# Kernel optimization log

Hardware: AMD Instinct MI355X
Metric: run time of the kernel (lower is better)

## Reference

```python
import jax, jax.numpy as jnp
import numpy as np
from jax import lax

B, N, C_IN, C_OUT = 4, 8192, 64, 128
STRIDE, RADIUS, K, L = 4, 0.1, 32, 2
EPS = 1e-5
M = N // STRIDE


def _bn(x, g, b):
    # training-mode batch norm, channel-first layout (B, C, ...)
    axes = (0,) + tuple(range(2, x.ndim))
    mean = jnp.mean(x, axis=axes, keepdims=True)
    var = jnp.mean((x - mean) ** 2, axis=axes, keepdims=True)
    sh = (1, -1) + (1,) * (x.ndim - 2)
    return (x - mean) * lax.rsqrt(var + EPS) * g.reshape(sh) + b.reshape(sh)


def _fps(points, m):
    # farthest point sampling starting at index 0 (matches fps_cuda semantics)
    b, n, _ = points.shape
    bi = jnp.arange(b)

    def body(carry, _):
        dis, last = carry
        lp = points[bi, last]  # (b,3)
        d = jnp.sum((points - lp[:, None, :]) ** 2, -1)
        dis = jnp.minimum(dis, d)
        return (dis, jnp.argmax(dis, -1).astype(jnp.int32)), last

    init = (jnp.full((b, n), 1e10, points.dtype), jnp.zeros((b,), jnp.int32))
    _, idx = lax.scan(body, init, None, length=m)
    return idx.T  # (b, m)


def _ball_query(radius, k, centroids, points, features):
    # first k points within radius of each centroid; pad with first hit
    b, n, _ = points.shape
    d2 = jnp.sum((centroids[:, :, None, :] - points[:, None, :, :]) ** 2, -1)  # (b,m,n)
    key = jnp.where(d2 < radius * radius, jnp.arange(n, dtype=jnp.int32), n)
    neg, _ = lax.top_k(-key, k)  # k smallest keys = first k in-ball indices
    sel = -neg  # (b,m,k)
    sel = jnp.where(sel == n, sel[..., :1], sel)
    sel = jnp.clip(sel, 0, n - 1)
    bi = jnp.arange(b)[:, None, None]
    gp = jnp.transpose(points[bi, sel], (0, 3, 2, 1))  # (b,3,k,m)
    gf = None
    if features is not None:
        gf = jnp.transpose(features[bi, sel], (0, 3, 2, 1))  # (b,c,k,m)
    return gp, gf


def _forward(pos, x, p):
    b, n, _ = pos.shape
    m = n // STRIDE
    bi = jnp.arange(b)[:, None]
    fps_idx = _fps(pos, m)
    centroids = pos[bi, fps_idx]  # (b,m,3)
    # x_mlp: 1x1 conv + BN + ReLU
    f = jax.nn.relu(_bn(jnp.einsum('bnc,oc->bon', x, p['W_x']), p['g_x'], p['b_x']))
    feats = jnp.transpose(f, (0, 2, 1))  # (b,n,C_OUT)
    gp, gf = _ball_query(RADIUS, K, centroids, pos, feats)
    cT = jnp.transpose(centroids, (0, 2, 1))[:, :, None, :]  # (b,3,1,m)
    gp = (gp - cT) / RADIUS
    gp = jax.nn.relu(_bn(jnp.einsum('bckm,oc->bokm', gp, p['W_ps']), p['g_ps'], p['b_ps']))
    xf = jnp.transpose(jnp.max(gf + gp, axis=2), (0, 2, 1))  # (b,m,C_OUT)
    # gen_pe on downsampled points
    R2 = RADIUS * 2
    gpe, _ = _ball_query(R2, K, centroids, centroids, None)
    gpe = (gpe - cT) / R2
    pe = jax.nn.relu(_bn(jnp.einsum('bckm,oc->bokm', gpe, p['W_pe']), p['g_pe'], p['b_pe']))
    # InvResMLP blocks
    for i in range(L):
        xc = jnp.transpose(xf, (0, 2, 1))  # (b,C,m)
        xc = jax.nn.relu(_bn(jnp.einsum('bcm,oc->bom', xc, p['W1'][i]), p['g1'][i], p['b1'][i]))
        feats_i = jnp.transpose(xc, (0, 2, 1))  # (b,m,C)
        _, gfi = _ball_query(R2, K, centroids, centroids, feats_i)
        g = jnp.max(gfi + pe, axis=2)  # (b,C,m)
        g = jax.nn.relu(_bn(jnp.einsum('bcm,oc->bom', g, p['W2a'][i]), p['g2a'][i], p['b2a'][i]))
        g = _bn(jnp.einsum('bcm,oc->bom', g, p['W2b'][i]), p['g2b'][i], p['b2b'][i])
        xf = jax.nn.relu(feats_i + jnp.transpose(g, (0, 2, 1)))
    return centroids, xf


def setup_inputs() -> dict:
    key = jax.random.key(0)
    ks = jax.random.split(key, 12)
    d = {
        'pos': jax.random.uniform(ks[0], (B, N, 3), jnp.float32),
        'x': jax.random.normal(ks[1], (B, N, C_IN), jnp.float32),
        'W_x': jax.random.normal(ks[2], (C_OUT, C_IN), jnp.float32) * 0.05,
        'g_x': jnp.ones((C_OUT,), jnp.float32), 'b_x': jnp.zeros((C_OUT,), jnp.float32),
        'W_ps': jax.random.normal(ks[3], (C_OUT, 3), jnp.float32) * 0.1,
        'g_ps': jnp.ones((C_OUT,), jnp.float32), 'b_ps': jnp.zeros((C_OUT,), jnp.float32),
        'W_pe': jax.random.normal(ks[4], (C_OUT, 3), jnp.float32) * 0.1,
        'g_pe': jnp.ones((C_OUT,), jnp.float32), 'b_pe': jnp.zeros((C_OUT,), jnp.float32),
        'W1': jax.random.normal(ks[5], (L, C_OUT, C_OUT), jnp.float32) * 0.05,
        'g1': jnp.ones((L, C_OUT), jnp.float32), 'b1': jnp.zeros((L, C_OUT), jnp.float32),
        'W2a': jax.random.normal(ks[6], (L, C_OUT, C_OUT), jnp.float32) * 0.05,
        'g2a': jnp.ones((L, C_OUT), jnp.float32), 'b2a': jnp.zeros((L, C_OUT), jnp.float32),
        'W2b': jax.random.normal(ks[7], (L, C_OUT, C_OUT), jnp.float32) * 0.05,
        'g2b': jnp.ones((L, C_OUT), jnp.float32), 'b2b': jnp.zeros((L, C_OUT), jnp.float32),
    }
    return d


def reference(pos, x, W_x, g_x, b_x, W_ps, g_ps, b_ps, W_pe, g_pe, b_pe,
              W1, g1, b1, W2a, g2a, b2a, W2b, g2b, b2b):
    p = dict(W_x=W_x, g_x=g_x, b_x=b_x, W_ps=W_ps, g_ps=g_ps, b_ps=b_ps,
             W_pe=W_pe, g_pe=g_pe, b_pe=b_pe, W1=W1, g1=g1, b1=b1,
             W2a=W2a, g2a=g2a, b2a=b2a, W2b=W2b, g2b=g2b, b2b=b2b)
    return _forward(pos, x, p)
```

## Files before the change

kernel.cpp:

```cpp
#include <hip/hip_runtime.h>


#define BB 4
#define NN 8192
#define MM 2048
#define HM 1024
#define KK 32
#define CI 64
#define CO 128
#define SG 16
#define CAPH 192

typedef float vf2 __attribute__((ext_vector_type(2)));

#define ST_X 0
#define MO_PS 256
#define MO_PE 272
#define ST1 288
#define ST2A (288 + 2 * SG * 256)
#define ST2B (ST2A + 2 * SG * 256)
#define ST_TOTAL (ST2B + 512)

__device__ __forceinline__ float sq3(float dx, float dy, float dz) {
#pragma clang fp contract(off)
  return dx * dx + dy * dy + dz * dz;
}

__device__ __forceinline__ void fin_stats_d(const double* st, float gam,
                                            float bet, double cnt, int ch,
                                            float* sc, float* sh) {
  double mean = st[ch] / cnt;
  double var = st[128 + ch] / cnt - mean * mean;
  if (var < 0) var = 0;
  double s = (double)gam / sqrt(var + 1e-5);
  *sc = (float)s;
  *sh = (float)((double)bet - mean * s);
}

__device__ __forceinline__ void fin_grp_d(const double* st, float gam,
                                          float bet, double cnt, int ch,
                                          float* sc, float* sh) {
  double sum = 0, ssq = 0;
#pragma unroll
  for (int g = 0; g < SG; g++) {
    sum += st[g * 256 + ch];
    ssq += st[g * 256 + 128 + ch];
  }
  double mean = sum / cnt;
  double var = ssq / cnt - mean * mean;
  if (var < 0) var = 0;
  double s = (double)gam / sqrt(var + 1e-5);
  *sc = (float)s;
  *sh = (float)((double)bet - mean * s);
}

__device__ __forceinline__ void fin_mom_d(const double* mo, const float* Wrow,
                                          float gam, float bet, double cnt,
                                          float* sc, float* sh) {
  double w0 = Wrow[0], w1 = Wrow[1], w2 = Wrow[2];
  double mx = mo[0] / cnt, my = mo[1] / cnt, mz = mo[2] / cnt;
  double sxx = mo[3] / cnt, sxy = mo[4] / cnt, sxz = mo[5] / cnt;
  double syy = mo[6] / cnt, syz = mo[7] / cnt, szz = mo[8] / cnt;
  double mean = w0 * mx + w1 * my + w2 * mz;
  double ey2 = w0 * w0 * sxx + w1 * w1 * syy + w2 * w2 * szz +
               2.0 * (w0 * w1 * sxy + w0 * w2 * sxz + w1 * w2 * syz);
  double var = ey2 - mean * mean;
  if (var < 0) var = 0;
  double s = (double)gam / sqrt(var + 1e-5);
  *sc = (float)s;
  *sh = (float)((double)bet - mean * s);
}

template <int CTRL>
__device__ __forceinline__ int dpp_i(int v) {
  return __builtin_amdgcn_update_dpp(v, v, CTRL, 0xF, 0xF, false);
}
template <int CTRL>
__device__ __forceinline__ float dpp_f(float v) {
  return __int_as_float(dpp_i<CTRL>(__float_as_int(v)));
}

#define FT 512
#define NP 8
#define NW 8

__device__ __forceinline__ void bq_grid(
    int pair, const float* __restrict__ pts, int npts,
    const float4* __restrict__ gxyz, const int* __restrict__ gstart, int G,
    float gs, float rad, float rsq, float inv_r, int* __restrict__ sel,
    const float* __restrict__ cent, int lane, int* __restrict__ s_hitw,
    int* __restrict__ s_selw, float* __restrict__ s_momw) {
  const float* C = cent + (size_t)pair * 3;
  float cx = C[0], cy = C[1], cz = C[2];
  unsigned long long ltm = (1ull << lane) - 1ull;
  int x0 = (int)((cx - rad - 1e-5f) * gs); x0 = x0 < 0 ? 0 : x0;
  int x1 = (int)((cx + rad + 1e-5f) * gs); x1 = x1 > G - 1 ? G - 1 : x1;
  int y0 = (int)((cy - rad - 1e-5f) * gs); y0 = y0 < 0 ? 0 : y0;
  int y1 = (int)((cy + rad + 1e-5f) * gs); y1 = y1 > G - 1 ? G - 1 : y1;
  int z0 = (int)((cz - rad - 1e-5f) * gs); z0 = z0 < 0 ? 0 : z0;
  int z1 = (int)((cz + rad + 1e-5f) * gs); z1 = z1 > G - 1 ? G - 1 : z1;
  int cnt = 0;
  for (int zz = z0; zz <= z1; zz++) {
    for (int yy = y0; yy <= y1; yy++) {
      int brow = (zz * G + yy) * G;
      int sbeg = gstart[brow + x0];
      int send = gstart[brow + x1 + 1];
      for (int base = sbeg; base < send; base += 64) {
        int j = base + lane;
        bool h = false;
        int pi = 0;
        if (j < send) {
          float4 v = gxyz[j];
          pi = __float_as_int(v.w);
          h = sq3(v.x - cx, v.y - cy, v.z - cz) < rsq;
        }
        unsigned long long mb = __ballot(h);
        if (mb) {
          int k = cnt + __popcll(mb & ltm);
          if (h && k < CAPH) s_hitw[k] = pi;
          cnt += __popcll(mb);
        }
      }
    }
  }
  __syncthreads();
  int total;
  if (cnt <= CAPH) {
    for (int l = lane; l < cnt; l += 64) {
      int v = s_hitw[l];
      int rk = 0;
      for (int j = 0; j < cnt; j++) rk += (s_hitw[j] < v);
      if (rk < KK) s_selw[rk] = v;
    }
    total = cnt < KK ? cnt : KK;
  } else {
    int bcnt = 0;
    int nit = npts >> 6;
    for (int ch = 0; ch < nit; ch++) {
      int i0 = (ch << 6) + lane;
      float a0 = pts[i0 * 3 + 0], a1 = pts[i0 * 3 + 1], a2 = pts[i0 * 3 + 2];
      bool h = sq3(a0 - cx, a1 - cy, a2 - cz) < rsq;
      unsigned long long mb = __ballot(h);
      if (mb) {
        int k = bcnt + __popcll(mb & ltm);
        if (h && k < KK) s_selw[k] = i0;
        bcnt += __popcll(mb);
      }
      if (bcnt >= KK) break;
    }
    total = bcnt < KK ? bcnt : KK;
  }
  __syncthreads();
  int myidx = 0;
  if (lane < KK) {
    int v = (lane < total) ? s_selw[lane] : s_selw[0];
    sel[(size_t)pair * KK + lane] = v;
    myidx = v;
  }
  float gx = 0.f, gy = 0.f, gz = 0.f;
  if (lane < KK) {
    gx = (pts[myidx * 3 + 0] - cx) * inv_r;
    gy = (pts[myidx * 3 + 1] - cy) * inv_r;
    gz = (pts[myidx * 3 + 2] - cz) * inv_r;
  }
  float v9[9] = {gx, gy, gz, gx * gx, gx * gy, gx * gz, gy * gy, gy * gz,
                 gz * gz};
#pragma unroll
  for (int j = 0; j < 9; j++) {
#pragma unroll
    for (int off = 32; off > 0; off >>= 1) v9[j] += __shfl_xor(v9[j], off);
  }
  if (lane == 0) {
#pragma unroll
    for (int j = 0; j < 9; j++) s_momw[j] = v9[j];
  }
}

__global__ __launch_bounds__(FT) void k_fps_conv(
    const float* __restrict__ pos, const float* __restrict__ x,
    const float* __restrict__ W_x, float* __restrict__ cent,
    float* __restrict__ fpre, double* __restrict__ stats,
    float* __restrict__ gds, int* __restrict__ pg_start,
    float4* __restrict__ pg_xyz) {
  __shared__ alignas(16) unsigned long long s_key[2][NW];
  __shared__ alignas(16) float s_pts[NN * 3];
  __shared__ alignas(16) float s_cent[MM * 3];
  int t = threadIdx.x;
  if (blockIdx.x >= BB + 256) {
    int bb = blockIdx.x - (BB + 256);
    const float* P = pos + (size_t)bb * NN * 3;
    int* cb = (int*)s_pts;
    int* rb = cb + 1024;
    for (int i = t; i < 1000; i += FT) cb[i] = 0;
    __syncthreads();
    for (int i = t; i < NN; i += FT) {
      float px = P[i * 3 + 0], py = P[i * 3 + 1], pz = P[i * 3 + 2];
      int bx = (int)(px * 10.f); bx = bx > 9 ? 9 : bx;
      int by = (int)(py * 10.f); by = by > 9 ? 9 : by;
      int bz = (int)(pz * 10.f); bz = bz > 9 ? 9 : bz;
      atomicAdd(&cb[(bz * 10 + by) * 10 + bx], 1);
    }
    __syncthreads();
    if (t == 0) {
      int acc = 0;
      for (int j = 0; j < 1000; j++) {
        pg_start[bb * 1024 + j] = acc;
        rb[j] = acc;
        acc += cb[j];
      }
      pg_start[bb * 1024 + 1000] = acc;
    }
    __syncthreads();
    for (int i = t; i < NN; i += FT) {
      float px = P[i * 3 + 0], py = P[i * 3 + 1], pz = P[i * 3 + 2];
      int bx = (int)(px * 10.f); bx = bx > 9 ? 9 : bx;
      int by = (int)(py * 10.f); by = by > 9 ? 9 : by;
      int bz = (int)(pz * 10.f); bz = bz > 9 ? 9 : bz;
      int slot = atomicAdd(&rb[(bz * 10 + by) * 10 + bx], 1);
      float4 v;
      v.x = px; v.y = py; v.z = pz; v.w = __int_as_float(i);
      pg_xyz[(size_t)bb * NN + slot] = v;
    }
    return;
  }
  if (blockIdx.x >= BB) {
    int cb2 = blockIdx.x - BB;
    int o = t & 127, q = t >> 7;
    float4 w[CI / 4];
    const float4* Wv = (const float4*)(W_x + (size_t)o * CI);
#pragma unroll
    for (int i = 0; i < CI / 4; i++) w[i] = Wv[i];
    int row0 = cb2 * 128;
    float ssum = 0.f, ssq = 0.f;
    for (int r = 0; r < 128; r += 4) {
      int row = __builtin_amdgcn_readfirstlane(row0 + r + q);
      const float* xr = x + (size_t)row * CI;
      float acc = 0.f;
#pragma unroll
      for (int i = 0; i < CI / 4; i++) {
        float4 a = *(const float4*)(xr + 4 * i);
        acc += a.x * w[i].x + a.y * w[i].y + a.z * w[i].z + a.w * w[i].w;
      }
      fpre[(size_t)row * CO + o] = acc;
      ssum += acc;
      ssq += acc * acc;
    }
    atomicAdd(&stats[ST_X + o], (double)ssum);
    atomicAdd(&stats[ST_X + 128 + o], (double)ssq);
    return;
  }
  int b = blockIdx.x;
  const float* P = pos + (size_t)b * NN * 3;
  float* C = cent + (size_t)b * MM * 3;
  int lane = t & 63, w = t >> 6;
  int ws = __builtin_amdgcn_readfirstlane(w);
  for (int i = t; i < (NN * 3) / 4; i += FT) {
    ((float4*)s_pts)[i] = ((const float4*)P)[i];
  }
  vf2 px[NP], py[NP], pz[NP], ds[NP];
#pragma unroll
  for (int s = 0; s < NP; s++) {
    int ia = (2 * s) * FT + t;
    int ib = ia + FT;
    px[s] = (vf2){P[ia * 3 + 0], P[ib * 3 + 0]};
    py[s] = (vf2){P[ia * 3 + 1], P[ib * 3 + 1]};
    pz[s] = (vf2){P[ia * 3 + 2], P[ib * 3 + 2]};
    ds[s] = (vf2){1e10f, 1e10f};
  }
  float lx = P[0], ly = P[1], lz = P[2];
  if (t == 0) {
    s_cent[0] = lx;
    s_cent[1] = ly;
    s_cent[2] = lz;
  }
  __syncthreads();
  for (int m = 1; m < HM; m++) {
    vf2 l2x = (vf2){lx, lx}, l2y = (vf2){ly, ly}, l2z = (vf2){lz, lz};
    vf2 bmax = (vf2){-1.0f, -1.0f};
    {
#pragma clang fp contract(off)
#pragma unroll
      for (int s = 0; s < NP; s++) {
        vf2 dx = px[s] - l2x;
        vf2 dy = py[s] - l2y;
        vf2 dz = pz[s] - l2z;
        vf2 d2 = dx * dx + dy * dy + dz * dz;
        vf2 nd = __builtin_elementwise_min(ds[s], d2);
        ds[s] = nd;
        bmax = __builtin_elementwise_max(bmax, nd);
      }
    }
    float bv = fmaxf(bmax.x, bmax.y);
    bv = fmaxf(bv, dpp_f<0x111>(bv));
    bv = fmaxf(bv, dpp_f<0x112>(bv));
    bv = fmaxf(bv, dpp_f<0x114>(bv));
    bv = fmaxf(bv, dpp_f<0x118>(bv));
    bv = fmaxf(bv, dpp_f<0x142>(bv));
    bv = fmaxf(bv, dpp_f<0x143>(bv));
    float wmax =
        __int_as_float(__builtin_amdgcn_readlane(__float_as_int(bv), 63));
    unsigned idxw = 0xffffffffu;
#pragma unroll
    for (int s = NP - 1; s >= 0; s--) {
      unsigned long long mby = __ballot(ds[s].y == wmax);
      unsigned basey = (unsigned)((2 * s) * FT + FT + (ws << 6));
      if (mby) idxw = basey + (unsigned)(__ffsll((long long)mby) - 1);
      unsigned long long mbx = __ballot(ds[s].x == wmax);
      unsigned basex = (unsigned)((2 * s) * FT + (ws << 6));
      if (mbx) idxw = basex + (unsigned)(__ffsll((long long)mbx) - 1);
    }
    int pb = m & 1;
    if (lane == 0) {
      s_key[pb][ws] = ((unsigned long long)__float_as_uint(wmax) << 32) |
                      (unsigned long long)(~idxw);
    }
    __syncthreads();
    const ulonglong2* kp = (const ulonglong2*)(&s_key[pb][0]);
    ulonglong2 q0 = kp[0];
    ulonglong2 q1 = kp[1];
    ulonglong2 q2 = kp[2];
    ulonglong2 q3 = kp[3];
    unsigned long long a0 = q0.x > q0.y ? q0.x : q0.y;
    unsigned long long a1 = q1.x > q1.y ? q1.x : q1.y;
    unsigned long long a2 = q2.x > q2.y ? q2.x : q2.y;
    unsigned long long a3 = q3.x > q3.y ? q3.x : q3.y;
    a0 = a0 > a1 ? a0 : a1;
    a2 = a2 > a3 ? a2 : a3;
    unsigned long long kw = a0 > a2 ? a0 : a2;
    unsigned gidx = ~(unsigned)(kw & 0xffffffffull);
    lx = s_pts[gidx * 3 + 0];
    ly = s_pts[gidx * 3 + 1];
    lz = s_pts[gidx * 3 + 2];
    if (t == 0) {
      s_cent[m * 3 + 0] = lx;
      s_cent[m * 3 + 1] = ly;
      s_cent[m * 3 + 2] = lz;
    }
  }
  __syncthreads();
  for (int i = t; i < (HM * 3) / 4; i += FT) {
    ((float4*)C)[i] = ((const float4*)s_cent)[i];
  }
  float2* gd = (float2*)gds + (size_t)b * NP * FT;
#pragma unroll
  for (int s = 0; s < NP; s++) {
    float2 v;
    v.x = ds[s].x;
    v.y = ds[s].y;
    gd[s * FT + t] = v;
  }
}

__global__ __launch_bounds__(FT) void k_fps_bq(
    const float* __restrict__ pos, float* __restrict__ cent,
    const float* __restrict__ gds, int* __restrict__ sel1,
    double* __restrict__ stats, const int* __restrict__ pg_start,
    const float4* __restrict__ pg_xyz) {
  __shared__ alignas(16) unsigned long long s_key[2][NW];
  __shared__ alignas(16) float s_pts[NN * 3];
  __shared__ alignas(16) float s_cent[MM * 3];
  __shared__ int s_hit[NW][CAPH];
  __shared__ int s_sel[NW][KK];
  __shared__ float s_mom[NW][9];
  int t = threadIdx.x;
  int lane = t & 63, w = t >> 6;
  if (blockIdx.x >= BB) {
    int pi = (blockIdx.x - BB) * 8 + w;
    int bb = pi >> 10, mi = pi & (HM - 1);
    int pair = bb * MM + mi;
    bq_grid(pair, pos + (size_t)bb * NN * 3, NN, pg_xyz + (size_t)bb * NN,
            pg_start + bb * 1024, 10, 10.f, 0.1f, 0.01f, 10.f, sel1, cent,
            lane, s_hit[w], s_sel[w], s_mom[w]);
    __syncthreads();
    if (t < 9) {
      double a = (double)s_mom[0][t];
#pragma unroll
      for (int j = 1; j < NW; j++) a += s_mom[j][t];
      atomicAdd(&stats[MO_PS + t], a);
    }
    return;
  }
  int b = blockIdx.x;
  const float* P = pos + (size_t)b * NN * 3;
  float* C = cent + (size_t)b * MM * 3;
  int ws = __builtin_amdgcn_readfirstlane(w);
  for (int i = t; i < (NN * 3) / 4; i += FT) {
    ((float4*)s_pts)[i] = ((const float4*)P)[i];
  }
  vf2 px[NP], py[NP], pz[NP], ds[NP];
  const float2* gd = (const float2*)gds + (size_t)b * NP * FT;
#pragma unroll
  for (int s = 0; s < NP; s++) {
    int ia = (2 * s) * FT + t;
    int ib = ia + FT;
    px[s] = (vf2){P[ia * 3 + 0], P[ib * 3 + 0]};
    py[s] = (vf2){P[ia * 3 + 1], P[ib * 3 + 1]};
    pz[s] = (vf2){P[ia * 3 + 2], P[ib * 3 + 2]};
    float2 v = gd[s * FT + t];
    ds[s] = (vf2){v.x, v.y};
  }
  float lx = C[(HM - 1) * 3 + 0];
  float ly = C[(HM - 1) * 3 + 1];
  float lz = C[(HM - 1) * 3 + 2];
  __syncthreads();
  for (int m = HM; m < MM; m++) {
    vf2 l2x = (vf2){lx, lx}, l2y = (vf2){ly, ly}, l2z = (vf2){lz, lz};
    vf2 bmax = (vf2){-1.0f, -1.0f};
    {
#pragma clang fp contract(off)
#pragma unroll
      for (int s = 0; s < NP; s++) {
        vf2 dx = px[s] - l2x;
        vf2 dy = py[s] - l2y;
        vf2 dz = pz[s] - l2z;
        vf2 d2 = dx * dx + dy * dy + dz * dz;
        vf2 nd = __builtin_elementwise_min(ds[s], d2);
        ds[s] = nd;
        bmax = __builtin_elementwise_max(bmax, nd);
      }
    }
    float bv = fmaxf(bmax.x, bmax.y);
    bv = fmaxf(bv, dpp_f<0x111>(bv));
    bv = fmaxf(bv, dpp_f<0x112>(bv));
    bv = fmaxf(bv, dpp_f<0x114>(bv));
    bv = fmaxf(bv, dpp_f<0x118>(bv));
    bv = fmaxf(bv, dpp_f<0x142>(bv));
    bv = fmaxf(bv, dpp_f<0x143>(bv));
    float wmax =
        __int_as_float(__builtin_amdgcn_readlane(__float_as_int(bv), 63));
    unsigned idxw = 0xffffffffu;
#pragma unroll
    for (int s = NP - 1; s >= 0; s--) {
      unsigned long long mby = __ballot(ds[s].y == wmax);
      unsigned basey = (unsigned)((2 * s) * FT + FT + (ws << 6));
      if (mby) idxw = basey + (unsigned)(__ffsll((long long)mby) - 1);
      unsigned long long mbx = __ballot(ds[s].x == wmax);
      unsigned basex = (unsigned)((2 * s) * FT + (ws << 6));
      if (mbx) idxw = basex + (unsigned)(__ffsll((long long)mbx) - 1);
    }
    int pb = m & 1;
    if (lane == 0) {
      s_key[pb][ws] = ((unsigned long long)__float_as_uint(wmax) << 32) |
                      (unsigned long long)(~idxw);
    }
    __syncthreads();
    const ulonglong2* kp = (const ulonglong2*)(&s_key[pb][0]);
    ulonglong2 q0 = kp[0];
    ulonglong2 q1 = kp[1];
    ulonglong2 q2 = kp[2];
    ulonglong2 q3 = kp[3];
    unsigned long long a0 = q0.x > q0.y ? q0.x : q0.y;
    unsigned long long a1 = q1.x > q1.y ? q1.x : q1.y;
    unsigned long long a2 = q2.x > q2.y ? q2.x : q2.y;
    unsigned long long a3 = q3.x > q3.y ? q3.x : q3.y;
    a0 = a0 > a1 ? a0 : a1;
    a2 = a2 > a3 ? a2 : a3;
    unsigned long long kw = a0 > a2 ? a0 : a2;
    unsigned gidx = ~(unsigned)(kw & 0xffffffffull);
    lx = s_pts[gidx * 3 + 0];
    ly = s_pts[gidx * 3 + 1];
    lz = s_pts[gidx * 3 + 2];
    if (t == 0) {
      s_cent[m * 3 + 0] = lx;
      s_cent[m * 3 + 1] = ly;
      s_cent[m * 3 + 2] = lz;
    }
  }
  __syncthreads();
  for (int i = t + (HM * 3) / 4; i < (MM * 3) / 4; i += FT) {
    ((float4*)C)[i] = ((const float4*)s_cent)[i];
  }
}

__global__ __launch_bounds__(256) void k_bin_cent(const float* __restrict__ cent,
                                                  int* __restrict__ cg_start,
                                                  float4* __restrict__ cg_xyz) {
  __shared__ int cb[128], rb[128];
  int t = threadIdx.x, bb = blockIdx.x;
  const float* C = cent + (size_t)bb * MM * 3;
  for (int i = t; i < 125; i += 256) cb[i] = 0;
  __syncthreads();
  for (int i = t; i < MM; i += 256) {
    float px = C[i * 3 + 0], py = C[i * 3 + 1], pz = C[i * 3 + 2];
    int bx = (int)(px * 5.f); bx = bx > 4 ? 4 : bx;
    int by = (int)(py * 5.f); by = by > 4 ? 4 : by;
    int bz = (int)(pz * 5.f); bz = bz > 4 ? 4 : bz;
    atomicAdd(&cb[(bz * 5 + by) * 5 + bx], 1);
  }
  __syncthreads();
  if (t == 0) {
    int acc = 0;
    for (int j = 0; j < 125; j++) {
      cg_start[bb * 128 + j] = acc;
      rb[j] = acc;
      acc += cb[j];
    }
    cg_start[bb * 128 + 125] = acc;
  }
  __syncthreads();
  for (int i = t; i < MM; i += 256) {
    float px = C[i * 3 + 0], py = C[i * 3 + 1], pz = C[i * 3 + 2];
    int bx = (int)(px * 5.f); bx = bx > 4 ? 4 : bx;
    int by = (int)(py * 5.f); by = by > 4 ? 4 : by;
    int bz = (int)(pz * 5.f); bz = bz > 4 ? 4 : bz;
    int slot = atomicAdd(&rb[(bz * 5 + by) * 5 + bx], 1);
    float4 v;
    v.x = px; v.y = py; v.z = pz; v.w = __int_as_float(i);
    cg_xyz[(size_t)bb * MM + slot] = v;
  }
}

__global__ __launch_bounds__(256) void k_bq_rest(
    const float* __restrict__ pos, const float* __restrict__ cent,
    const int* __restrict__ pg_start, const float4* __restrict__ pg_xyz,
    const int* __restrict__ cg_start, const float4* __restrict__ cg_xyz,
    int* __restrict__ sel1, int* __restrict__ sel2,
    double* __restrict__ stats) {
  __shared__ int s_hit[4][CAPH];
  __shared__ int s_sel[4][KK];
  __shared__ float s_mom[4][9];
  int t = threadIdx.x, lane = t & 63, w = t >> 6;
  int mo;
  if (blockIdx.x < (BB * (MM - HM)) / 4) {
    int pi = blockIdx.x * 4 + w;
    int bb = pi >> 10;
    int mi = (pi & (HM - 1)) + HM;
    int pair = bb * MM + mi;
    bq_grid(pair, pos + (size_t)bb * NN * 3, NN, pg_xyz + (size_t)bb * NN,
            pg_start + bb * 1024, 10, 10.f, 0.1f, 0.01f, 10.f, sel1, cent,
            lane, s_hit[w], s_sel[w], s_mom[w]);
    mo = MO_PS;
  } else {
    int pi = (blockIdx.x - (BB * (MM - HM)) / 4) * 4 + w;
    int bb = pi >> 11;
    bq_grid(pi, cent + (size_t)bb * MM * 3, MM, cg_xyz + (size_t)bb * MM,
            cg_start + bb * 128, 5, 5.f, 0.2f, 0.04f, 5.f, sel2, cent, lane,
            s_hit[w], s_sel[w], s_mom[w]);
    mo = MO_PE;
  }
  __syncthreads();
  if (t < 9) {
    double a = (double)s_mom[0][t] + s_mom[1][t] + s_mom[2][t] + s_mom[3][t];
    atomicAdd(&stats[mo + t], a);
  }
}

__global__ __launch_bounds__(512) void k_xf_conv1(
    const float* __restrict__ pos, const float* __restrict__ cent,
    const int* __restrict__ sel1, const float* __restrict__ fpre,
    const float* __restrict__ Wps, const float* __restrict__ g_ps,
    const float* __restrict__ b_ps, const float* __restrict__ g_x,
    const float* __restrict__ b_x, const double* __restrict__ stats,
    const float* __restrict__ W1, float* __restrict__ y1a,
    double* __restrict__ st1out) {
  __shared__ alignas(16) float s_sx[128], s_hx[128], s_sp[128], s_hp[128];
  __shared__ alignas(16) float s_w0[128], s_w1[128], s_w2[128];
  __shared__ alignas(16) int s_idx[4][KK];
  __shared__ alignas(16) float s_xf[4][128];
  __shared__ alignas(16) double s_rs[4][128], s_rq[4][128];
  int t = threadIdx.x, bid = blockIdx.x;
  if (t < 128) {
    float sx, hx, sp, hp;
    fin_stats_d(stats + ST_X, g_x[t], b_x[t], (double)(BB * NN), t, &sx, &hx);
    fin_mom_d(stats + MO_PS, Wps + t * 3, g_ps[t], b_ps[t],
              (double)(BB * MM * KK), &sp, &hp);
    s_sx[t] = sx;
    s_hx[t] = hx;
    s_sp[t] = sp;
    s_hp[t] = hp;
    s_w0[t] = Wps[t * 3 + 0];
    s_w1[t] = Wps[t * 3 + 1];
    s_w2[t] = Wps[t * 3 + 2];
  }
  __syncthreads();
  int o = t & 127, sub = t >> 7;
  float sx = s_sx[o], hx = s_hx[o], sp = s_sp[o], hp = s_hp[o];
  float w0 = s_w0[o], w1 = s_w1[o], w2 = s_w2[o];
  double rsum = 0.0, rsq = 0.0;
  for (int p = 0; p < 8; p++) {
    int pair = bid * 32 + p * 4 + sub;
    int b = pair >> 11;
    const float* C = cent + (size_t)pair * 3;
    float cx = C[0], cy = C[1], cz = C[2];
    const float* P = pos + (size_t)b * NN * 3;
    const float* F = fpre + (size_t)b * NN * CO;
    if (o < KK) s_idx[sub][o] = sel1[(size_t)pair * KK + o];
    __syncthreads();
    float acc = -1e30f;
#pragma unroll 4
    for (int k = 0; k < KK; k++) {
      int idx = __builtin_amdgcn_readfirstlane(s_idx[sub][k]);
      float gx = (P[idx * 3 + 0] - cx) * 10.0f;
      float gy = (P[idx * 3 + 1] - cy) * 10.0f;
      float gz = (P[idx * 3 + 2] - cz) * 10.0f;
      float y = fmaxf((w0 * gx + w1 * gy + w2 * gz) * sp + hp, 0.f);
      float f = fmaxf(F[(size_t)idx * CO + o] * sx + hx, 0.f);
      float v = y + f;
      acc = v > acc ? v : acc;
    }
    s_xf[sub][o] = acc;
    __syncthreads();
    const float4* Wv = (const float4*)(W1 + (size_t)o * CO);
    const float4* gv = (const float4*)(&s_xf[sub][0]);
    float dot = 0.f;
#pragma unroll
    for (int i = 0; i < CO / 4; i++) {
      float4 a = gv[i];
      float4 ww = Wv[i];
      dot += a.x * ww.x + a.y * ww.y + a.z * ww.z + a.w * ww.w;
    }
    y1a[(size_t)pair * CO + o] = dot;
    rsum += (double)dot;
    rsq += (double)(dot * dot);
  }
  s_rs[sub][o] = rsum;
  s_rq[sub][o] = rsq;
  __syncthreads();
  int grp = bid & (SG - 1);
  if (t < 128) {
    double a = s_rs[0][t] + s_rs[1][t] + s_rs[2][t] + s_rs[3][t];
    atomicAdd(&st1out[grp * 256 + t], a);
  } else if (t < 256) {
    int c = t - 128;
    double a = s_rq[0][c] + s_rq[1][c] + s_rq[2][c] + s_rq[3][c];
    atomicAdd(&st1out[grp * 256 + 128 + c], a);
  }
}

__global__ __launch_bounds__(256) void k_conv_bnin(
    const float* __restrict__ in, const float* __restrict__ W,
    const double* __restrict__ st_grp, const float* __restrict__ gam,
    const float* __restrict__ bet, float* __restrict__ out,
    double* __restrict__ stats, int rows_per_block) {
  __shared__ float s_sc[128], s_sh[128];
  int t = threadIdx.x;
  if (t < 128) {
    fin_grp_d(st_grp, gam[t], bet[t], (double)(BB * MM), t, &s_sc[t],
              &s_sh[t]);
  }
  __syncthreads();
  int o = t & 127, half = t >> 7;
  float4 w[CO / 4];
  const float4* Wv = (const float4*)(W + (size_t)o * CO);
#pragma unroll
  for (int i = 0; i < CO / 4; i++) w[i] = Wv[i];
  int row0 = blockIdx.x * rows_per_block;
  float ssum = 0.f, ssq = 0.f;
  for (int r = 0; r < rows_per_block; r += 2) {
    int row = __builtin_amdgcn_readfirstlane(row0 + r + half);
    const float* xr = in + (size_t)row * CO;
    float acc = 0.f;
#pragma unroll
    for (int i = 0; i < CO / 4; i++) {
      float4 a = *(const float4*)(xr + 4 * i);
      a.x = fmaxf(a.x * s_sc[4 * i + 0] + s_sh[4 * i + 0], 0.f);
      a.y = fmaxf(a.y * s_sc[4 * i + 1] + s_sh[4 * i + 1], 0.f);
      a.z = fmaxf(a.z * s_sc[4 * i + 2] + s_sh[4 * i + 2], 0.f);
      a.w = fmaxf(a.w * s_sc[4 * i + 3] + s_sh[4 * i + 3], 0.f);
      acc += a.x * w[i].x + a.y * w[i].y + a.z * w[i].z + a.w * w[i].w;
    }
    out[(size_t)row * CO + o] = acc;
    ssum += acc;
    ssq += acc * acc;
  }
  atomicAdd(&stats[o], (double)ssum);
  atomicAdd(&stats[128 + o], (double)ssq);
}

__global__ __launch_bounds__(256) void k_conv_resid(
    const float* __restrict__ y1prev, const float* __restrict__ y2bprev,
    const double* __restrict__ st1p, const float* __restrict__ g1p,
    const float* __restrict__ b1p, const double* __restrict__ st2bp,
    const float* __restrict__ g2bp, const float* __restrict__ b2bp,
    const float* __restrict__ W, float* __restrict__ y1out,
    double* __restrict__ stats, int rows_per_block) {
  __shared__ float s_s1[128], s_h1[128], s_s2[128], s_h2[128];
  int t = threadIdx.x;
  if (t < 128) {
    fin_grp_d(st1p, g1p[t], b1p[t], (double)(BB * MM), t, &s_s1[t], &s_h1[t]);
    fin_stats_d(st2bp, g2bp[t], b2bp[t], (double)(BB * MM), t, &s_s2[t],
                &s_h2[t]);
  }
  __syncthreads();
  int o = t & 127, half = t >> 7;
  float4 w[CO / 4];
  const float4* Wv = (const float4*)(W + (size_t)o * CO);
#pragma unroll
  for (int i = 0; i < CO / 4; i++) w[i] = Wv[i];
  int row0 = blockIdx.x * rows_per_block;
  float ssum = 0.f, ssq = 0.f;
  for (int r = 0; r < rows_per_block; r += 2) {
    int row = __builtin_amdgcn_readfirstlane(row0 + r + half);
    const float* ar = y1prev + (size_t)row * CO;
    const float* br = y2bprev + (size_t)row * CO;
    float acc = 0.f;
#pragma unroll
    for (int i = 0; i < CO / 4; i++) {
      float4 a = *(const float4*)(ar + 4 * i);
      float4 bb = *(const float4*)(br + 4 * i);
      float x0 = fmaxf(fmaxf(a.x * s_s1[4 * i + 0] + s_h1[4 * i + 0], 0.f) +
                           (bb.x * s_s2[4 * i + 0] + s_h2[4 * i + 0]), 0.f);
      float x1 = fmaxf(fmaxf(a.y * s_s1[4 * i + 1] + s_h1[4 * i + 1], 0.f) +
                           (bb.y * s_s2[4 * i + 1] + s_h2[4 * i + 1]), 0.f);
      float x2 = fmaxf(fmaxf(a.z * s_s1[4 * i + 2] + s_h1[4 * i + 2], 0.f) +
                           (bb.z * s_s2[4 * i + 2] + s_h2[4 * i + 2]), 0.f);
      float x3 = fmaxf(fmaxf(a.w * s_s1[4 * i + 3] + s_h1[4 * i + 3], 0.f) +
                           (bb.w * s_s2[4 * i + 3] + s_h2[4 * i + 3]), 0.f);
      acc += x0 * w[i].x + x1 * w[i].y + x2 * w[i].z + x3 * w[i].w;
    }
    y1out[(size_t)row * CO + o] = acc;
    ssum += acc;
    ssq += acc * acc;
  }
  int grp = blockIdx.x & (SG - 1);
  atomicAdd(&stats[grp * 256 + o], (double)ssum);
  atomicAdd(&stats[grp * 256 + 128 + o], (double)ssq);
}

__global__ __launch_bounds__(512) void k_gconv(
    const float* __restrict__ cent, const int* __restrict__ sel2,
    const float* __restrict__ y1in, const double* __restrict__ st1,
    const float* __restrict__ g1v, const float* __restrict__ b1v,
    const double* __restrict__ mo_pe, const float* __restrict__ Wpe,
    const float* __restrict__ gpe, const float* __restrict__ bpe,
    const float* __restrict__ W2a, float* __restrict__ y2a,
    double* __restrict__ st2a) {
  __shared__ alignas(16) float s_s1[128], s_h1[128], s_se[128], s_he[128];
  __shared__ alignas(16) float s_w0[128], s_w1[128], s_w2[128];
  __shared__ alignas(16) int s_idx[4][KK];
  __shared__ alignas(16) float s_g[4][128];
  __shared__ alignas(16) double s_rs[4][128], s_rq[4][128];
  int t = threadIdx.x, bid = blockIdx.x;
  if (t < 128) {
    float s1, h1, se, he;
    fin_grp_d(st1, g1v[t], b1v[t], (double)(BB * MM), t, &s1, &h1);
    fin_mom_d(mo_pe, Wpe + t * 3, gpe[t], bpe[t], (double)(BB * MM * KK), &se,
              &he);
    s_s1[t] = s1;
    s_h1[t] = h1;
    s_se[t] = se;
    s_he[t] = he;
    s_w0[t] = Wpe[t * 3 + 0];
    s_w1[t] = Wpe[t * 3 + 1];
    s_w2[t] = Wpe[t * 3 + 2];
  }
  __syncthreads();
  int o = t & 127, sub = t >> 7;
  float s1 = s_s1[o], h1 = s_h1[o], se = s_se[o], he = s_he[o];
  float w0 = s_w0[o], w1 = s_w1[o], w2 = s_w2[o];
  double rsum = 0.0, rsq = 0.0;
  for (int p = 0; p < 8; p++) {
    int pair = bid * 32 + p * 4 + sub;
    int b = pair >> 11;
    const float* C = cent + (size_t)pair * 3;
    float cx = C[0], cy = C[1], cz = C[2];
    const float* CB = cent + (size_t)b * MM * 3;
    const float* Y = y1in + (size_t)b * MM * CO;
    if (o < KK) s_idx[sub][o] = sel2[(size_t)pair * KK + o];
    __syncthreads();
    float acc = -1e30f;
#pragma unroll 4
    for (int k = 0; k < KK; k++) {
      int idx = __builtin_amdgcn_readfirstlane(s_idx[sub][k]);
      float gx = (CB[idx * 3 + 0] - cx) * 5.0f;
      float gy = (CB[idx * 3 + 1] - cy) * 5.0f;
      float gz = (CB[idx * 3 + 2] - cz) * 5.0f;
      float pe = fmaxf((w0 * gx + w1 * gy + w2 * gz) * se + he, 0.f);
      float f = fmaxf(Y[(size_t)idx * CO + o] * s1 + h1, 0.f);
      float v = pe + f;
      acc = v > acc ? v : acc;
    }
    s_g[sub][o] = acc;
    __syncthreads();
    const float4* Wv = (const float4*)(W2a + (size_t)o * CO);
    const float4* gv = (const float4*)(&s_g[sub][0]);
    float dot = 0.f;
#pragma unroll
    for (int i = 0; i < CO / 4; i++) {
      float4 a = gv[i];
      float4 ww = Wv[i];
      dot += a.x * ww.x + a.y * ww.y + a.z * ww.z + a.w * ww.w;
    }
    y2a[(size_t)pair * CO + o] = dot;
    rsum += (double)dot;
    rsq += (double)(dot * dot);
  }
  s_rs[sub][o] = rsum;
  s_rq[sub][o] = rsq;
  __syncthreads();
  int grp = bid & (SG - 1);
  if (t < 128) {
    double a = s_rs[0][t] + s_rs[1][t] + s_rs[2][t] + s_rs[3][t];
    atomicAdd(&st2a[grp * 256 + t], a);
  } else if (t < 256) {
    int c = t - 128;
    double a = s_rq[0][c] + s_rq[1][c] + s_rq[2][c] + s_rq[3][c];
    atomicAdd(&st2a[grp * 256 + 128 + c], a);
  }
}

__global__ __launch_bounds__(256) void k_resid_fin(
    const float* __restrict__ y1b, const double* __restrict__ st1,
    const float* __restrict__ g1v, const float* __restrict__ b1v,
    const float* __restrict__ y2b, const double* __restrict__ st2b,
    const float* __restrict__ g2bv, const float* __restrict__ b2bv,
    float* __restrict__ xf) {
  int i = blockIdx.x * 256 + threadIdx.x;
  int o = i & 127;
  float s1, h1, s2, h2;
  fin_grp_d(st1, g1v[o], b1v[o], (double)(BB * MM), o, &s1, &h1);
  fin_stats_d(st2b, g2bv[o], b2bv[o], (double)(BB * MM), o, &s2, &h2);
  float f = fmaxf(y1b[i] * s1 + h1, 0.f);
  float v = y2b[i] * s2 + h2;
  xf[i] = fmaxf(f + v, 0.f);
}

extern "C" void kernel_launch(void* const* d_in, const int* in_sizes, int n_in,
                              void* d_out, int out_size, void* d_ws,
                              size_t ws_size, hipStream_t stream) {
  const float* pos = (const float*)d_in[0];
  const float* x = (const float*)d_in[1];
  const float* W_x = (const float*)d_in[2];
  const float* g_x = (const float*)d_in[3];
  const float* b_x = (const float*)d_in[4];
  const float* W_ps = (const float*)d_in[5];
  const float* g_ps = (const float*)d_in[6];
  const float* b_ps = (const float*)d_in[7];
  const float* W_pe = (const float*)d_in[8];
  const float* g_pe = (const float*)d_in[9];
  const float* b_pe = (const float*)d_in[10];
  const float* W1 = (const float*)d_in[11];
  const float* g1 = (const float*)d_in[12];
  const float* b1 = (const float*)d_in[13];
  const float* W2a = (const float*)d_in[14];
  const float* g2a = (const float*)d_in[15];
  const float* b2a = (const float*)d_in[16];
  const float* W2b = (const float*)d_in[17];
  const float* g2b = (const float*)d_in[18];
  const float* b2b = (const float*)d_in[19];

  float* cent = (float*)d_out;
  float* xf = cent + (size_t)BB * MM * 3;

  char* p = (char*)d_ws;
  double* stats = (double*)p; p += (size_t)ST_TOTAL * sizeof(double);
  int* sel1 = (int*)p;        p += (size_t)BB * MM * KK * sizeof(int);
  int* sel2 = (int*)p;        p += (size_t)BB * MM * KK * sizeof(int);
  float* fpre = (float*)p;    p += (size_t)BB * NN * CO * sizeof(float);
  float* y1a = (float*)p;     p += (size_t)BB * MM * CO * sizeof(float);
  float* y1b = (float*)p;     p += (size_t)BB * MM * CO * sizeof(float);
  float* y2a = (float*)p;     p += (size_t)BB * MM * CO * sizeof(float);
  float* y2b = (float*)p;     p += (size_t)BB * MM * CO * sizeof(float);
  float* gds = (float*)p;     p += (size_t)BB * NP * FT * 2 * sizeof(float);
  float4* pg_xyz = (float4*)p; p += (size_t)BB * NN * sizeof(float4);
  float4* cg_xyz = (float4*)p; p += (size_t)BB * MM * sizeof(float4);
  int* pg_start = (int*)p;    p += (size_t)BB * 1024 * sizeof(int);
  int* cg_start = (int*)p;    p += (size_t)BB * 128 * sizeof(int);

  hipMemsetAsync(stats, 0, (size_t)ST_TOTAL * sizeof(double), stream);
  k_fps_conv<<<BB + 256 + BB, FT, 0, stream>>>(pos, x, W_x, cent, fpre, stats,
                                               gds, pg_start, pg_xyz);
  k_fps_bq<<<BB + (BB * HM) / 8, FT, 0, stream>>>(pos, cent, gds, sel1, stats,
                                                  pg_start, pg_xyz);
  k_bin_cent<<<BB, 256, 0, stream>>>(cent, cg_start, cg_xyz);
  k_bq_rest<<<(BB * (MM - HM)) / 4 + (BB * MM) / 4, 256, 0, stream>>>(
      pos, cent, pg_start, pg_xyz, cg_start, cg_xyz, sel1, sel2, stats);
  k_xf_conv1<<<256, 512, 0, stream>>>(pos, cent, sel1, fpre, W_ps, g_ps,
                                      b_ps, g_x, b_x, stats, W1, y1a,
                                      stats + ST1);
  k_gconv<<<256, 512, 0, stream>>>(cent, sel2, y1a, stats + ST1, g1, b1,
                                   stats + MO_PE, W_pe, g_pe, b_pe, W2a, y2a,
                                   stats + ST2A);
  k_conv_bnin<<<128, 256, 0, stream>>>(y2a, W2b, stats + ST2A, g2a, b2a, y2b,
                                       stats + ST2B, 64);
  k_conv_resid<<<128, 256, 0, stream>>>(
      y1a, y2b, stats + ST1, g1, b1, stats + ST2B, g2b, b2b, W1 + CO * CO, y1b,
      stats + ST1 + SG * 256, 64);
  k_gconv<<<256, 512, 0, stream>>>(cent, sel2, y1b, stats + ST1 + SG * 256,
                                   g1 + 128, b1 + 128, stats + MO_PE, W_pe,
                                   g_pe, b_pe, W2a + CO * CO, y2a,
                                   stats + ST2A + SG * 256);
  k_conv_bnin<<<128, 256, 0, stream>>>(y2a, W2b + CO * CO,
                                       stats + ST2A + SG * 256, g2a + 128,
                                       b2a + 128, y2b, stats + ST2B + 256, 64);
  k_resid_fin<<<(BB * MM * CO) / 256, 256, 0, stream>>>(
      y1b, stats + ST1 + SG * 256, g1 + 128, b1 + 128, y2b,
      stats + ST2B + 256, g2b + 128, b2b + 128, xf);
}
```

Measured before the change: 2.464 ms.

## Use spatially binned point order in FPS and skip waves via bounding-box bound

Moves the point binning into its own kernel launched before FPS, so each FPS thread loads points in grid-cell order and spatially nearby points land in the same wave. Each wave computes a bounding box of its points, and on each iteration skips the distance update when the box's lower-bound distance to the new centroid cannot beat the wave's current max. Argmax tie-breaking switches from ballots to a DPP min reduction over original indices packed as 16-bit IDs. This adds an extra kernel launch and serializes binning before FPS, and the skip branch causes divergence between waves but not within one.

```diff
diff --git a/kernel.cpp b/kernel.cpp
--- a/kernel.cpp
+++ b/kernel.cpp
@@ -78,6 +78,34 @@
 template <int CTRL>
 __device__ __forceinline__ float dpp_f(float v) {
   return __int_as_float(dpp_i<CTRL>(__float_as_int(v)));
+}
+__device__ __forceinline__ float wave_fmax63(float v) {
+  v = fmaxf(v, dpp_f<0x111>(v));
+  v = fmaxf(v, dpp_f<0x112>(v));
+  v = fmaxf(v, dpp_f<0x114>(v));
+  v = fmaxf(v, dpp_f<0x118>(v));
+  v = fmaxf(v, dpp_f<0x142>(v));
+  v = fmaxf(v, dpp_f<0x143>(v));
+  return v;
+}
+__device__ __forceinline__ float wave_fmin63(float v) {
+  v = fminf(v, dpp_f<0x111>(v));
+  v = fminf(v, dpp_f<0x112>(v));
+  v = fminf(v, dpp_f<0x114>(v));
+  v = fminf(v, dpp_f<0x118>(v));
+  v = fminf(v, dpp_f<0x142>(v));
+  v = fminf(v, dpp_f<0x143>(v));
+  return v;
+}
+__device__ __forceinline__ unsigned wave_umin63(unsigned v) {
+  unsigned u;
+  u = (unsigned)dpp_i<0x111>((int)v); v = u < v ? u : v;
+  u = (unsigned)dpp_i<0x112>((int)v); v = u < v ? u : v;
+  u = (unsigned)dpp_i<0x114>((int)v); v = u < v ? u : v;
+  u = (unsigned)dpp_i<0x118>((int)v); v = u < v ? u : v;
+  u = (unsigned)dpp_i<0x142>((int)v); v = u < v ? u : v;
+  u = (unsigned)dpp_i<0x143>((int)v); v = u < v ? u : v;
+  return v;
 }
 
 #define FT 512
@@ -176,53 +204,53 @@
   }
 }
 
+__global__ __launch_bounds__(FT) void k_bin_pos(const float* __restrict__ pos,
+                                                int* __restrict__ pg_start,
+                                                float4* __restrict__ pg_xyz) {
+  __shared__ int cb[1024], rb[1024];
+  int t = threadIdx.x, bb = blockIdx.x;
+  const float* P = pos + (size_t)bb * NN * 3;
+  for (int i = t; i < 1000; i += FT) cb[i] = 0;
+  __syncthreads();
+  for (int i = t; i < NN; i += FT) {
+    float px = P[i * 3 + 0], py = P[i * 3 + 1], pz = P[i * 3 + 2];
+    int bx = (int)(px * 10.f); bx = bx > 9 ? 9 : bx;
+    int by = (int)(py * 10.f); by = by > 9 ? 9 : by;
+    int bz = (int)(pz * 10.f); bz = bz > 9 ? 9 : bz;
+    atomicAdd(&cb[(bz * 10 + by) * 10 + bx], 1);
+  }
+  __syncthreads();
+  if (t == 0) {
+    int acc = 0;
+    for (int j = 0; j < 1000; j++) {
+      pg_start[bb * 1024 + j] = acc;
+      rb[j] = acc;
+      acc += cb[j];
+    }
+    pg_start[bb * 1024 + 1000] = acc;
+  }
+  __syncthreads();
+  for (int i = t; i < NN; i += FT) {
+    float px = P[i * 3 + 0], py = P[i * 3 + 1], pz = P[i * 3 + 2];
+    int bx = (int)(px * 10.f); bx = bx > 9 ? 9 : bx;
+    int by = (int)(py * 10.f); by = by > 9 ? 9 : by;
+    int bz = (int)(pz * 10.f); bz = bz > 9 ? 9 : bz;
+    int slot = atomicAdd(&rb[(bz * 10 + by) * 10 + bx], 1);
+    float4 v;
+    v.x = px; v.y = py; v.z = pz; v.w = __int_as_float(i);
+    pg_xyz[(size_t)bb * NN + slot] = v;
+  }
+}
+
 __global__ __launch_bounds__(FT) void k_fps_conv(
     const float* __restrict__ pos, const float* __restrict__ x,
     const float* __restrict__ W_x, float* __restrict__ cent,
     float* __restrict__ fpre, double* __restrict__ stats,
-    float* __restrict__ gds, int* __restrict__ pg_start,
-    float4* __restrict__ pg_xyz) {
+    float* __restrict__ gds, const float4* __restrict__ pg_xyz) {
   __shared__ alignas(16) unsigned long long s_key[2][NW];
   __shared__ alignas(16) float s_pts[NN * 3];
   __shared__ alignas(16) float s_cent[MM * 3];
   int t = threadIdx.x;
-  if (blockIdx.x >= BB + 256) {
-    int bb = blockIdx.x - (BB + 256);
-    const float* P = pos + (size_t)bb * NN * 3;
-    int* cb = (int*)s_pts;
-    int* rb = cb + 1024;
-    for (int i = t; i < 1000; i += FT) cb[i] = 0;
-    __syncthreads();
-    for (int i = t; i < NN; i += FT) {
-      float px = P[i * 3 + 0], py = P[i * 3 + 1], pz = P[i * 3 + 2];
-      int bx = (int)(px * 10.f); bx = bx > 9 ? 9 : bx;
-      int by = (int)(py * 10.f); by = by > 9 ? 9 : by;
-      int bz = (int)(pz * 10.f); bz = bz > 9 ? 9 : bz;
-      atomicAdd(&cb[(bz * 10 + by) * 10 + bx], 1);
-    }
-    __syncthreads();
-    if (t == 0) {
-      int acc = 0;
-      for (int j = 0; j < 1000; j++) {
-        pg_start[bb * 1024 + j] = acc;
-        rb[j] = acc;
-        acc += cb[j];
-      }
-      pg_start[bb * 1024 + 1000] = acc;
-    }
-    __syncthreads();
-    for (int i = t; i < NN; i += FT) {
-      float px = P[i * 3 + 0], py = P[i * 3 + 1], pz = P[i * 3 + 2];
-      int bx = (int)(px * 10.f); bx = bx > 9 ? 9 : bx;
-      int by = (int)(py * 10.f); by = by > 9 ? 9 : by;
-      int bz = (int)(pz * 10.f); bz = bz > 9 ? 9 : bz;
-      int slot = atomicAdd(&rb[(bz * 10 + by) * 10 + bx], 1);
-      float4 v;
-      v.x = px; v.y = py; v.z = pz; v.w = __int_as_float(i);
-      pg_xyz[(size_t)bb * NN + slot] = v;
-    }
-    return;
-  }
   if (blockIdx.x >= BB) {
     int cb2 = blockIdx.x - BB;
     int o = t & 127, q = t >> 7;
@@ -251,6 +279,7 @@
   }
   int b = blockIdx.x;
   const float* P = pos + (size_t)b * NN * 3;
+  const float4* G = pg_xyz + (size_t)b * NN;
   float* C = cent + (size_t)b * MM * 3;
   int lane = t & 63, w = t >> 6;
   int ws = __builtin_amdgcn_readfirstlane(w);
@@ -258,15 +287,45 @@
     ((float4*)s_pts)[i] = ((const float4*)P)[i];
   }
   vf2 px[NP], py[NP], pz[NP], ds[NP];
+  unsigned oid[NP];
 #pragma unroll
   for (int s = 0; s < NP; s++) {
     int ia = (2 * s) * FT + t;
     int ib = ia + FT;
-    px[s] = (vf2){P[ia * 3 + 0], P[ib * 3 + 0]};
-    py[s] = (vf2){P[ia * 3 + 1], P[ib * 3 + 1]};
-    pz[s] = (vf2){P[ia * 3 + 2], P[ib * 3 + 2]};
+    float4 va = G[ia];
+    float4 vb = G[ib];
+    px[s] = (vf2){va.x, vb.x};
+    py[s] = (vf2){va.y, vb.y};
+    pz[s] = (vf2){va.z, vb.z};
+    oid[s] = ((unsigned)__float_as_int(va.w) & 0xffffu) |
+             ((unsigned)__float_as_int(vb.w) << 16);
     ds[s] = (vf2){1e10f, 1e10f};
   }
+  float mnx = 1e30f, mxx = -1e30f, mny = 1e30f, mxy = -1e30f;
+  float mnz = 1e30f, mxz = -1e30f;
+#pragma unroll
+  for (int s = 0; s < NP; s++) {
+    mnx = fminf(mnx, fminf(px[s].x, px[s].y));
+    mxx = fmaxf(mxx, fmaxf(px[s].x, px[s].y));
+    mny = fminf(mny, fminf(py[s].x, py[s].y));
+    mxy = fmaxf(mxy, fmaxf(py[s].x, py[s].y));
+    mnz = fminf(mnz, fminf(pz[s].x, pz[s].y));
+    mxz = fmaxf(mxz, fmaxf(pz[s].x, pz[s].y));
+  }
+  float bx0 = __int_as_float(
+      __builtin_amdgcn_readlane(__float_as_int(wave_fmin63(mnx)), 63));
+  float bx1 = __int_as_float(
+      __builtin_amdgcn_readlane(__float_as_int(wave_fmax63(mxx)), 63));
+  float by0 = __int_as_float(
+      __builtin_amdgcn_readlane(__float_as_int(wave_fmin63(mny)), 63));
+  float by1 = __int_as_float(
+      __builtin_amdgcn_readlane(__float_as_int(wave_fmax63(mxy)), 63));
+  float bz0 = __int_as_float(
+      __builtin_amdgcn_readlane(__float_as_int(wave_fmin63(mnz)), 63));
+  float bz1 = __int_as_float(
+      __builtin_amdgcn_readlane(__float_as_int(wave_fmax63(mxz)), 63));
+  float pwmax = 1e30f;
+  unsigned long long pkey = 0;
   float lx = P[0], ly = P[1], lz = P[2];
   if (t == 0) {
     s_cent[0] = lx;
@@ -275,44 +334,50 @@
   }
   __syncthreads();
   for (int m = 1; m < HM; m++) {
-    vf2 l2x = (vf2){lx, lx}, l2y = (vf2){ly, ly}, l2z = (vf2){lz, lz};
-    vf2 bmax = (vf2){-1.0f, -1.0f};
-    {
+    int pb = m & 1;
+    float qx = fminf(fmaxf(lx, bx0), bx1);
+    float qy = fminf(fmaxf(ly, by0), by1);
+    float qz = fminf(fmaxf(lz, bz0), bz1);
+    float lb2 = sq3(qx - lx, qy - ly, qz - lz);
+    if (lb2 >= pwmax) {
+      if (lane == 0) s_key[pb][ws] = pkey;
+    } else {
+      vf2 l2x = (vf2){lx, lx}, l2y = (vf2){ly, ly}, l2z = (vf2){lz, lz};
+      vf2 bmax = (vf2){-1.0f, -1.0f};
+      {
 #pragma clang fp contract(off)
 #pragma unroll
+        for (int s = 0; s < NP; s++) {
+          vf2 dx = px[s] - l2x;
+          vf2 dy = py[s] - l2y;
+          vf2 dz = pz[s] - l2z;
+          vf2 d2 = dx * dx + dy * dy + dz * dz;
+          vf2 nd = __builtin_elementwise_min(ds[s], d2);
+          ds[s] = nd;
+          bmax = __builtin_elementwise_max(bmax, nd);
+        }
+      }
+      float bv = wave_fmax63(fmaxf(bmax.x, bmax.y));
+      float wmax =
+          __int_as_float(__builtin_amdgcn_readlane(__float_as_int(bv), 63));
+      unsigned mi = 0xffffffffu;
+#pragma unroll
       for (int s = 0; s < NP; s++) {
-        vf2 dx = px[s] - l2x;
-        vf2 dy = py[s] - l2y;
-        vf2 dz = pz[s] - l2z;
-        vf2 d2 = dx * dx + dy * dy + dz * dz;
-        vf2 nd = __builtin_elementwise_min(ds[s], d2);
-        ds[s] = nd;
-        bmax = __builtin_elementwise_max(bmax, nd);
+        if (ds[s].x == wmax) {
+          unsigned a = oid[s] & 0xffffu;
+          mi = a < mi ? a : mi;
+        }
+        if (ds[s].y == wmax) {
+          unsigned a = oid[s] >> 16;
+          mi = a < mi ? a : mi;
+        }
       }
-    }
-    float bv = fmaxf(bmax.x, bmax.y);
-    bv = fmaxf(bv, dpp_f<0x111>(bv));
-    bv = fmaxf(bv, dpp_f<0x112>(bv));
-    bv = fmaxf(bv, dpp_f<0x114>(bv));
-    bv = fmaxf(bv, dpp_f<0x118>(bv));
-    bv = fmaxf(bv, dpp_f<0x142>(bv));
-    bv = fmaxf(bv, dpp_f<0x143>(bv));
-    float wmax =
-        __int_as_float(__builtin_amdgcn_readlane(__float_as_int(bv), 63));
-    unsigned idxw = 0xffffffffu;
-#pragma unroll
-    for (int s = NP - 1; s >= 0; s--) {
-      unsigned long long mby = __ballot(ds[s].y == wmax);
-      unsigned basey = (unsigned)((2 * s) * FT + FT + (ws << 6));
-      if (mby) idxw = basey + (unsigned)(__ffsll((long long)mby) - 1);
-      unsigned long long mbx = __ballot(ds[s].x == wmax);
-      unsigned basex = (unsigned)((2 * s) * FT + (ws << 6));
-      if (mbx) idxw = basex + (unsigned)(__ffsll((long long)mbx) - 1);
-    }
-    int pb = m & 1;
-    if (lane == 0) {
-      s_key[pb][ws] = ((unsigned long long)__float_as_uint(wmax) << 32) |
-                      (unsigned long long)(~idxw);
+      mi = wave_umin63(mi);
+      unsigned miw = (unsigned)__builtin_amdgcn_readlane((int)mi, 63);
+      pwmax = wmax;
+      pkey = ((unsigned long long)__float_as_uint(wmax) << 32) |
+             (unsigned long long)(~miw);
+      if (lane == 0) s_key[pb][ws] = pkey;
     }
     __syncthreads();
     const ulonglong2* kp = (const ulonglong2*)(&s_key[pb][0]);
@@ -382,66 +447,103 @@
   }
   int b = blockIdx.x;
   const float* P = pos + (size_t)b * NN * 3;
+  const float4* G = pg_xyz + (size_t)b * NN;
   float* C = cent + (size_t)b * MM * 3;
   int ws = __builtin_amdgcn_readfirstlane(w);
   for (int i = t; i < (NN * 3) / 4; i += FT) {
     ((float4*)s_pts)[i] = ((const float4*)P)[i];
   }
   vf2 px[NP], py[NP], pz[NP], ds[NP];
+  unsigned oid[NP];
   const float2* gd = (const float2*)gds + (size_t)b * NP * FT;
 #pragma unroll
   for (int s = 0; s < NP; s++) {
     int ia = (2 * s) * FT + t;
     int ib = ia + FT;
-    px[s] = (vf2){P[ia * 3 + 0], P[ib * 3 + 0]};
-    py[s] = (vf2){P[ia * 3 + 1], P[ib * 3 + 1]};
-    pz[s] = (vf2){P[ia * 3 + 2], P[ib * 3 + 2]};
+    float4 va = G[ia];
+    float4 vb = G[ib];
+    px[s] = (vf2){va.x, vb.x};
+    py[s] = (vf2){va.y, vb.y};
+    pz[s] = (vf2){va.z, vb.z};
+    oid[s] = ((unsigned)__float_as_int(va.w) & 0xffffu) |
+             ((unsigned)__float_as_int(vb.w) << 16);
     float2 v = gd[s * FT + t];
     ds[s] = (vf2){v.x, v.y};
   }
+  float mnx = 1e30f, mxx = -1e30f, mny = 1e30f, mxy = -1e30f;
+  float mnz = 1e30f, mxz = -1e30f;
+#pragma unroll
+  for (int s = 0; s < NP; s++) {
+    mnx = fminf(mnx, fminf(px[s].x, px[s].y));
+    mxx = fmaxf(mxx, fmaxf(px[s].x, px[s].y));
+    mny = fminf(mny, fminf(py[s].x, py[s].y));
+    mxy = fmaxf(mxy, fmaxf(py[s].x, py[s].y));
+    mnz = fminf(mnz, fminf(pz[s].x, pz[s].y));
+    mxz = fmaxf(mxz, fmaxf(pz[s].x, pz[s].y));
+  }
+  float bx0 = __int_as_float(
+      __builtin_amdgcn_readlane(__float_as_int(wave_fmin63(mnx)), 63));
+  float bx1 = __int_as_float(
+      __builtin_amdgcn_readlane(__float_as_int(wave_fmax63(mxx)), 63));
+  float by0 = __int_as_float(
+      __builtin_amdgcn_readlane(__float_as_int(wave_fmin63(mny)), 63));
+  float by1 = __int_as_float(
+      __builtin_amdgcn_readlane(__float_as_int(wave_fmax63(mxy)), 63));
+  float bz0 = __int_as_float(
+      __builtin_amdgcn_readlane(__float_as_int(wave_fmin63(mnz)), 63));
+  float bz1 = __int_as_float(
+      __builtin_amdgcn_readlane(__float_as_int(wave_fmax63(mxz)), 63));
+  float pwmax = 1e30f;
+  unsigned long long pkey = 0;
   float lx = C[(HM - 1) * 3 + 0];
   float ly = C[(HM - 1) * 3 + 1];
   float lz = C[(HM - 1) * 3 + 2];
   __syncthreads();
   for (int m = HM; m < MM; m++) {
-    vf2 l2x = (vf2){lx, lx}, l2y = (vf2){ly, ly}, l2z = (vf2){lz, lz};
-    vf2 bmax = (vf2){-1.0f, -1.0f};
-    {
+    int pb = m & 1;
+    float qx = fminf(fmaxf(lx, bx0), bx1);
+    float qy = fminf(fmaxf(ly, by0), by1);
+    float qz = fminf(fmaxf(lz, bz0), bz1);
+    float lb2 = sq3(qx - lx, qy - ly, qz - lz);
+    if (lb2 >= pwmax) {
+      if (lane == 0) s_key[pb][ws] = pkey;
+    } else {
+      vf2 l2x = (vf2){lx, lx}, l2y = (vf2){ly, ly}, l2z = (vf2){lz, lz};
+      vf2 bmax = (vf2){-1.0f, -1.0f};
+      {
 #pragma clang fp contract(off)
 #pragma unroll
+        for (int s = 0; s < NP; s++) {
+          vf2 dx = px[s] - l2x;
+          vf2 dy = py[s] - l2y;
+          vf2 dz = pz[s] - l2z;
+          vf2 d2 = dx * dx + dy * dy + dz * dz;
+          vf2 nd = __builtin_elementwise_min(ds[s], d2);
+          ds[s] = nd;
+          bmax = __builtin_elementwise_max(bmax, nd);
+        }
+      }
+      float bv = wave_fmax63(fmaxf(bmax.x, bmax.y));
+      float wmax =
+          __int_as_float(__builtin_amdgcn_readlane(__float_as_int(bv), 63));
+      unsigned mi = 0xffffffffu;
+#pragma unroll
       for (int s = 0; s < NP; s++) {
-        vf2 dx = px[s] - l2x;
-        vf2 dy = py[s] - l2y;
-        vf2 dz = pz[s] - l2z;
-        vf2 d2 = dx * dx + dy * dy + dz * dz;
-        vf2 nd = __builtin_elementwise_min(ds[s], d2);
-        ds[s] = nd;
-        bmax = __builtin_elementwise_max(bmax, nd);
+        if (ds[s].x == wmax) {
+          unsigned a = oid[s] & 0xffffu;
+          mi = a < mi ? a : mi;
+        }
+        if (ds[s].y == wmax) {
+          unsigned a = oid[s] >> 16;
+          mi = a < mi ? a : mi;
+        }
       }
-    }
-    float bv = fmaxf(bmax.x, bmax.y);
-    bv = fmaxf(bv, dpp_f<0x111>(bv));
-    bv = fmaxf(bv, dpp_f<0x112>(bv));
-    bv = fmaxf(bv, dpp_f<0x114>(bv));
-    bv = fmaxf(bv, dpp_f<0x118>(bv));
-    bv = fmaxf(bv, dpp_f<0x142>(bv));
-    bv = fmaxf(bv, dpp_f<0x143>(bv));
-    float wmax =
-        __int_as_float(__builtin_amdgcn_readlane(__float_as_int(bv), 63));
-    unsigned idxw = 0xffffffffu;
-#pragma unroll
-    for (int s = NP - 1; s >= 0; s--) {
-      unsigned long long mby = __ballot(ds[s].y == wmax);
-      unsigned basey = (unsigned)((2 * s) * FT + FT + (ws << 6));
-      if (mby) idxw = basey + (unsigned)(__ffsll((long long)mby) - 1);
-      unsigned long long mbx = __ballot(ds[s].x == wmax);
-      unsigned basex = (unsigned)((2 * s) * FT + (ws << 6));
-      if (mbx) idxw = basex + (unsigned)(__ffsll((long long)mbx) - 1);
-    }
-    int pb = m & 1;
-    if (lane == 0) {
-      s_key[pb][ws] = ((unsigned long long)__float_as_uint(wmax) << 32) |
-                      (unsigned long long)(~idxw);
+      mi = wave_umin63(mi);
+      unsigned miw = (unsigned)__builtin_amdgcn_readlane((int)mi, 63);
+      pwmax = wmax;
+      pkey = ((unsigned long long)__float_as_uint(wmax) << 32) |
+             (unsigned long long)(~miw);
+      if (lane == 0) s_key[pb][ws] = pkey;
     }
     __syncthreads();
     const ulonglong2* kp = (const ulonglong2*)(&s_key[pb][0]);
@@ -858,8 +960,9 @@
   int* cg_start = (int*)p;    p += (size_t)BB * 128 * sizeof(int);
 
   hipMemsetAsync(stats, 0, (size_t)ST_TOTAL * sizeof(double), stream);
-  k_fps_conv<<<BB + 256 + BB, FT, 0, stream>>>(pos, x, W_x, cent, fpre, stats,
-                                               gds, pg_start, pg_xyz);
+  k_bin_pos<<<BB, FT, 0, stream>>>(pos, pg_start, pg_xyz);
+  k_fps_conv<<<BB + 256, FT, 0, stream>>>(pos, x, W_x, cent, fpre, stats, gds,
+                                          pg_xyz);
   k_fps_bq<<<BB + (BB * HM) / 8, FT, 0, stream>>>(pos, cent, gds, sel1, stats,
                                                   pg_start, pg_xyz);
   k_bin_cent<<<BB, 256, 0, stream>>>(cent, cg_start, cg_xyz);
```

After: 3.215 ms. 30.5% more time.
